# Kernel optimization log

Measured on AMD Instinct MI355X. Metric: run time of the kernel, lower is better.

Reference implementation:

```python
import jax, jax.numpy as jnp
import numpy as np

D_MODEL = 1024
NUM_HEADS = 16
DILATION = 2
SEGMENT = 2048


def setup_inputs() -> dict:
    key = jax.random.key(0)
    ks = jax.random.split(key, 5)
    B, S, D = 2, 8192, D_MODEL
    scale = 1.0 / np.sqrt(D)
    return {
        "x": jax.random.normal(ks[0], (B, S, D), dtype=jnp.float32),
        "Wqkv": jax.random.normal(ks[1], (D, 3 * D), dtype=jnp.float32) * scale,
        "bqkv": jax.random.normal(ks[2], (3 * D,), dtype=jnp.float32) * 0.01,
        "Wout": jax.random.normal(ks[3], (D, D), dtype=jnp.float32) * scale,
        "bout": jax.random.normal(ks[4], (D,), dtype=jnp.float32) * 0.01,
    }


def reference(x, Wqkv, bqkv, Wout, bout):
    B, S, D = x.shape
    H = NUM_HEADS
    hd = D // H
    n_seg = S // SEGMENT
    # view into segments, then dilated strided token selection within each segment
    xs = x.reshape(B, n_seg, SEGMENT, D)[:, :, ::DILATION, :]  # [B, n_seg, L, D]
    L = xs.shape[2]
    # fused QKV projection (FlashMHA)
    qkv = xs @ Wqkv + bqkv                                      # [B, n_seg, L, 3D]
    qkv = qkv.reshape(B, n_seg, L, 3, H, hd)
    q, k, v = qkv[..., 0, :, :], qkv[..., 1, :, :], qkv[..., 2, :, :]
    scores = jnp.einsum("bsqhd,bskhd->bshqk", q, k) / jnp.sqrt(jnp.asarray(hd, x.dtype))
    probs = jax.nn.softmax(scores, axis=-1)                     # [B, n_seg, H, L, L]
    ctx = jnp.einsum("bshqk,bskhd->bsqhd", probs, v)            # [B, n_seg, L, H, hd]
    ctx = ctx.reshape(B, n_seg, L, D)
    out = ctx @ Wout + bout                                     # [B, n_seg, L, D]
    # dropout p=0, casual=False, no rel-pos bias -> identity here
    return out.reshape(B, n_seg * L, D)                         # [B, S // DILATION, D]
```

## Files before the change

kernel.cpp:

```cpp
#include <hip/hip_runtime.h>
#include <hip/hip_bf16.h>

#define TOKENS  8192
#define QK_SC2  0.1803368801f

typedef short  short8 __attribute__((ext_vector_type(8)));
typedef float  f32x4  __attribute__((ext_vector_type(4)));
typedef float  f32x16 __attribute__((ext_vector_type(16)));
typedef unsigned short us4 __attribute__((ext_vector_type(4)));

__device__ __forceinline__ unsigned short f2bf_rne(float f) {
    unsigned u = __float_as_uint(f);
    unsigned r = (u + 0x7FFFu + ((u >> 16) & 1u)) >> 16;
    return (unsigned short)r;
}
__device__ __forceinline__ unsigned cvt_pk_bf16(float a, float b) {
    unsigned r;
    asm("v_cvt_pk_bf16_f32 %0, %1, %2" : "=v"(r) : "v"(a), "v"(b));
    return r;
}
__device__ __forceinline__ void permlane32_swap(unsigned &a, unsigned &b) {
    asm("v_permlane32_swap_b32 %0, %1" : "+v"(a), "+v"(b));
}
__device__ __forceinline__ void gld16(const void* gptr, void* lptr) {
    __builtin_amdgcn_global_load_lds(
        (const __attribute__((address_space(1))) void*)gptr,
        (__attribute__((address_space(3))) void*)lptr, 16, 0, 0);
}

__global__ __launch_bounds__(256)
void prep_x_kernel(const float* __restrict__ x, unsigned short* __restrict__ Ax)
{
    const int t = blockIdx.x;
    const int c = threadIdx.x * 4;
    const long xrow = (long)((t >> 10) * 2048 + (t & 1023) * 2);
    float4 v = *reinterpret_cast<const float4*>(&x[xrow * 1024 + c]);
    us4 hv;
    hv[0] = f2bf_rne(v.x);
    hv[1] = f2bf_rne(v.y);
    hv[2] = f2bf_rne(v.z);
    hv[3] = f2bf_rne(v.w);
    *reinterpret_cast<us4*>(&Ax[(size_t)t * 1024 + c]) = hv;
}

__global__ __launch_bounds__(256)
void prep_w_kernel(const float* __restrict__ W, unsigned short* __restrict__ Wt, int N)
{
    __shared__ float T[32][33];
    const int n0 = blockIdx.x * 32, k0 = blockIdx.y * 32;
    const int tid = threadIdx.x;
#pragma unroll
    for (int p = 0; p < 4; p++) {
        int r = p * 8 + (tid >> 5), c = tid & 31;
        T[r][c] = W[(long)(k0 + r) * N + n0 + c];
    }
    __syncthreads();
#pragma unroll
    for (int p = 0; p < 4; p++) {
        int on = p * 8 + (tid >> 5), ok = tid & 31;
        Wt[(size_t)(n0 + on) * 1024 + k0 + ok] = f2bf_rne(T[ok][on]);
    }
}

template<int EPI, int ASPLIT>
__global__ __launch_bounds__(512, 1)
void gemm2p_kernel(const unsigned short* __restrict__ A,
                   const unsigned short* __restrict__ Bt,
                   const float* __restrict__ bias,
                   float* __restrict__ C,
                   unsigned short* __restrict__ Qb,
                   unsigned short* __restrict__ Kb,
                   unsigned short* __restrict__ Vt,
                   int N, int NBX)
{
    __shared__ __align__(16) char lds[3 * 49152];

    const int NT = ASPLIT ? 32 : 16;
    const int ASTRIDE = ASPLIT ? 2048 : 1024;

    const int tid = threadIdx.x;
    const int l = tid & 63, w = tid >> 6;
    const int wm = w >> 2, wn = w & 3;
    const int l15 = l & 15;

    const int cpx = gridDim.x >> 3;
    const int wg = (blockIdx.x & 7) * cpx + (blockIdx.x >> 3);
    const int by = wg / NBX, bx = wg - by * NBX;
    const int trow0 = by * 128, col0 = bx * 256;

    size_t gOff[6];
    int    lOff[6];
    {
        const int c = tid & 7;
#pragma unroll
        for (int p = 0; p < 2; p++) {
            {
                const int row = (tid + p * 512) >> 3;
                const int cg = c ^ (row & 7);
                gOff[p] = (size_t)(trow0 + row) * ASTRIDE + cg * 8;
                lOff[p] = row * 128 + c * 16;
            }
            {
                const int u = (tid + p * 512) >> 3;
                const int row = ((u >> 5) << 6) + (u & 31);
                const int cg = c ^ (row & 7);
                gOff[2 + p] = (size_t)(col0 + row) * 1024 + cg * 8;
                lOff[2 + p] = 16384 + row * 128 + c * 16;
            }
            {
                const int u = (tid + p * 512) >> 3;
                const int row = ((u >> 5) << 6) + 32 + (u & 31);
                const int cg = c ^ (row & 7);
                gOff[4 + p] = (size_t)(col0 + row) * 1024 + cg * 8;
                lOff[4 + p] = 16384 + row * 128 + c * 16;
            }
        }
    }

    const int offs0 = (((l >> 4) * 16)     ) ^ ((l & 7) << 4);
    const int offs1 = (((l >> 4) * 16) + 64) ^ ((l & 7) << 4);

    f32x4 acc[4][4];
#pragma unroll
    for (int i = 0; i < 4; i++)
#pragma unroll
        for (int j = 0; j < 4; j++) acc[i][j] = (f32x4){0.f, 0.f, 0.f, 0.f};

#pragma unroll
    for (int t0 = 0; t0 < 2; ++t0) {
        char* buf = lds + t0 * 49152;
        const int ac = t0 * 64;
        gld16(&A [gOff[0] + ac], buf + lOff[0]);
        gld16(&A [gOff[1] + ac], buf + lOff[1]);
        gld16(&Bt[gOff[2] + ac], buf + lOff[2]);
        gld16(&Bt[gOff[3] + ac], buf + lOff[3]);
        gld16(&Bt[gOff[4] + ac], buf + lOff[4]);
        gld16(&Bt[gOff[5] + ac], buf + lOff[5]);
    }
    asm volatile("s_waitcnt vmcnt(6)" ::: "memory");
    __builtin_amdgcn_s_barrier();

    int bc3 = 0;
    for (int t = 0; t < NT; ++t) {
        char* buf = lds + bc3 * 49152;
        const int bn = (bc3 >= 1) ? bc3 - 1 : 2;
        char* nbuf = lds + bn * 49152;
        const int tp = t + 2;
        const bool pf = (tp < NT);
        const int ac  = pf ? (ASPLIT ? (((tp >> 4) ? 1024 : 0) + (tp & 15) * 64)
                                     : tp * 64) : 0;
        const int bcc = pf ? ((tp & 15) * 64) : 0;

        short8 af[4][2], bf0[2][2], bf1[2][2];
#pragma unroll
        for (int i = 0; i < 4; ++i) {
            const int r = wm * 64 + i * 16 + l15;
            af[i][0] = *reinterpret_cast<const short8*>(buf + r * 128 + offs0);
            af[i][1] = *reinterpret_cast<const short8*>(buf + r * 128 + offs1);
        }
#pragma unroll
        for (int j = 0; j < 2; ++j) {
            const int r = wn * 64 + j * 16 + l15;
            bf0[j][0] = *reinterpret_cast<const short8*>(buf + 16384 + r * 128 + offs0);
            bf0[j][1] = *reinterpret_cast<const short8*>(buf + 16384 + r * 128 + offs1);
        }
        if (pf) {
            gld16(&A [gOff[0] + ac],  nbuf + lOff[0]);
            gld16(&A [gOff[1] + ac],  nbuf + lOff[1]);
            gld16(&Bt[gOff[2] + bcc], nbuf + lOff[2]);
            gld16(&Bt[gOff[3] + bcc], nbuf + lOff[3]);
        }
        __builtin_amdgcn_s_barrier();
        __builtin_amdgcn_s_setprio(1);
#pragma unroll
        for (int i = 0; i < 4; ++i)
#pragma unroll
            for (int j = 0; j < 2; ++j) {
                acc[i][j] = __builtin_amdgcn_mfma_f32_16x16x32_bf16(
                    af[i][0], bf0[j][0], acc[i][j], 0, 0, 0);
                acc[i][j] = __builtin_amdgcn_mfma_f32_16x16x32_bf16(
                    af[i][1], bf0[j][1], acc[i][j], 0, 0, 0);
            }
        __builtin_amdgcn_s_setprio(0);
        __builtin_amdgcn_s_barrier();

#pragma unroll
        for (int j = 0; j < 2; ++j) {
            const int r = wn * 64 + 32 + j * 16 + l15;
            bf1[j][0] = *reinterpret_cast<const short8*>(buf + 16384 + r * 128 + offs0);
            bf1[j][1] = *reinterpret_cast<const short8*>(buf + 16384 + r * 128 + offs1);
        }
        if (pf) {
            gld16(&Bt[gOff[4] + bcc], nbuf + lOff[4]);
            gld16(&Bt[gOff[5] + bcc], nbuf + lOff[5]);
        }
        __builtin_amdgcn_s_barrier();
        __builtin_amdgcn_s_setprio(1);
#pragma unroll
        for (int i = 0; i < 4; ++i)
#pragma unroll
            for (int j = 0; j < 2; ++j) {
                acc[i][2 + j] = __builtin_amdgcn_mfma_f32_16x16x32_bf16(
                    af[i][0], bf1[j][0], acc[i][2 + j], 0, 0, 0);
                acc[i][2 + j] = __builtin_amdgcn_mfma_f32_16x16x32_bf16(
                    af[i][1], bf1[j][1], acc[i][2 + j], 0, 0, 0);
            }
        __builtin_amdgcn_s_setprio(0);

        if (pf) asm volatile("s_waitcnt vmcnt(6)" ::: "memory");
        else    asm volatile("s_waitcnt vmcnt(0)" ::: "memory");
        __builtin_amdgcn_s_barrier();

        bc3 = (bc3 >= 2) ? 0 : bc3 + 1;
    }

#pragma unroll
    for (int j = 0; j < 4; ++j) {
        const int gc = col0 + wn * 64 + j * 16 + l15;
        const float bv = bias[gc];
        if (EPI == 0) {
#pragma unroll
            for (int i = 0; i < 4; ++i) {
                const int gr0 = trow0 + wm * 64 + i * 16 + (l >> 4) * 4;
#pragma unroll
                for (int r = 0; r < 4; ++r)
                    C[(size_t)(gr0 + r) * N + gc] = acc[i][j][r] + bv;
            }
        } else {
            const int which = gc >> 10;
            const int head  = (gc >> 6) & 15;
            const int d     = gc & 63;
            if (which == 2) {
#pragma unroll
                for (int i = 0; i < 4; ++i) {
                    const int gr0 = trow0 + wm * 64 + i * 16 + (l >> 4) * 4;
                    const size_t base =
                        ((size_t)((gr0 >> 10) * 16 + head) << 16)
                        + (size_t)d * 1024 + (gr0 & 1023);
                    union { unsigned u[2]; us4 v; } pk;
                    pk.u[0] = cvt_pk_bf16(acc[i][j][0] + bv, acc[i][j][1] + bv);
                    pk.u[1] = cvt_pk_bf16(acc[i][j][2] + bv, acc[i][j][3] + bv);
                    *reinterpret_cast<us4*>(&Vt[base]) = pk.v;
                }
            } else {
                unsigned short* dst = (which == 0) ? Qb : Kb;
                const float sc = (which == 0) ? QK_SC2 : 1.f;
#pragma unroll
                for (int i = 0; i < 4; ++i) {
                    const int gr0 = trow0 + wm * 64 + i * 16 + (l >> 4) * 4;
                    const unsigned a01 = cvt_pk_bf16((acc[i][j][0] + bv) * sc,
                                                     (acc[i][j][1] + bv) * sc);
                    const unsigned a23 = cvt_pk_bf16((acc[i][j][2] + bv) * sc,
                                                     (acc[i][j][3] + bv) * sc);
                    const size_t adr0 = ((size_t)((gr0 >> 10) * 16 + head) << 16)
                                      + (size_t)(gr0 & 1023) * 64 + d;
                    dst[adr0]           = (unsigned short)a01;
                    dst[adr0 + 64]      = (unsigned short)(a01 >> 16);
                    dst[adr0 + 128]     = (unsigned short)a23;
                    dst[adr0 + 192]     = (unsigned short)(a23 >> 16);
                }
            }
        }
    }
}

__global__ __launch_bounds__(256)
void attn_mfma_kernel(const unsigned short* __restrict__ Qb,
                      const unsigned short* __restrict__ Kb,
                      const unsigned short* __restrict__ Vt,
                      unsigned short* __restrict__ ctx)
{
    __shared__ __align__(16) char Ks[2][8192];
    __shared__ __align__(16) char Vs[2][8192];

    const int id  = blockIdx.x;
    const int bsh = (id >> 6) * 8 + (id & 7);
    const int qc  = (id >> 3) & 7;
    const int bseg = bsh >> 4, h = bsh & 15;
    const int tid = threadIdx.x;
    const int w = tid >> 6, l = tid & 63;
    const int H = l >> 5, lq = l & 31;
    const int q0 = qc * 128 + w * 32;

    const size_t hbytes = (size_t)bsh << 17;

    int srowA[2], scolA[2], sdst[2];
#pragma unroll
    for (int p = 0; p < 2; p++) {
        const int c = w + p * 4;
        const int o = c * 1024 + l * 16;
        srowA[p] = o >> 7;
        scolA[p] = (o & 127) ^ ((l >> 3) << 4);
        sdst[p]  = c * 1024;
    }

    short8 qf[4];
    {
        const char* qsrc = (const char*)Qb + hbytes + (size_t)(q0 + lq) * 128;
#pragma unroll
        for (int ks = 0; ks < 4; ks++)
            qf[ks] = *reinterpret_cast<const short8*>(qsrc + ks * 32 + H * 16);
    }

    f32x16 o0, o1;
#pragma unroll
    for (int r = 0; r < 16; r++) { o0[r] = 0.f; o1[r] = 0.f; }
    float lsum = 0.f;

#pragma unroll
    for (int p = 0; p < 2; p++) {
        gld16((const char*)Kb + hbytes + (size_t)(srowA[p]) * 128 + scolA[p],
              Ks[0] + sdst[p]);
        gld16((const char*)Vt + hbytes + (size_t)srowA[p] * 2048 + scolA[p],
              Vs[0] + sdst[p]);
    }
    __syncthreads();

    for (int t = 0; t < 16; t++) {
        const int cur = t & 1;

        if (t + 1 < 16) {
            const int nb = cur ^ 1;
#pragma unroll
            for (int p = 0; p < 2; p++) {
                gld16((const char*)Kb + hbytes
                          + (size_t)((t + 1) * 64 + srowA[p]) * 128 + scolA[p],
                      Ks[nb] + sdst[p]);
                gld16((const char*)Vt + hbytes
                          + (size_t)srowA[p] * 2048 + (t + 1) * 128 + scolA[p],
                      Vs[nb] + sdst[p]);
            }
        }

        f32x16 s0, s1;
#pragma unroll
        for (int r = 0; r < 16; r++) { s0[r] = 0.f; s1[r] = 0.f; }
#pragma unroll
        for (int ks = 0; ks < 4; ks++) {
            const int b0 = (lq * 128 + ks * 32 + H * 16) ^ ((lq & 7) << 4);
            short8 k0 = *reinterpret_cast<const short8*>(Ks[cur] + b0);
            short8 k1 = *reinterpret_cast<const short8*>(Ks[cur] + b0 + 4096);
            s0 = __builtin_amdgcn_mfma_f32_32x32x16_bf16(k0, qf[ks], s0, 0, 0, 0);
            s1 = __builtin_amdgcn_mfma_f32_32x32x16_bf16(k1, qf[ks], s1, 0, 0, 0);
        }

        float pv[32];
        float ps = 0.f;
#pragma unroll
        for (int r = 0; r < 16; r++) {
            pv[r]      = __builtin_amdgcn_exp2f(s0[r]);
            pv[16 + r] = __builtin_amdgcn_exp2f(s1[r]);
        }
#pragma unroll
        for (int r = 0; r < 32; r++) ps += pv[r];
        lsum += ps;

#pragma unroll
        for (int kf = 0; kf < 2; kf++) {
            unsigned c8[8];
#pragma unroll
            for (int i = 0; i < 8; i++)
                c8[i] = cvt_pk_bf16(pv[kf * 16 + 2 * i], pv[kf * 16 + 2 * i + 1]);
#pragma unroll
            for (int tt = 0; tt < 2; tt++) {
                const int b = tt * 4;
                unsigned u0 = c8[b + 0], u2 = c8[b + 2];
                unsigned u1 = c8[b + 1], u3 = c8[b + 3];
                permlane32_swap(u0, u2);
                permlane32_swap(u1, u3);
                union { unsigned u[4]; short8 v; } pa;
                pa.u[0] = u0; pa.u[1] = u1; pa.u[2] = u2; pa.u[3] = u3;
                const int vb0 = (lq * 128 + kf * 64 + tt * 32 + H * 16) ^ ((lq & 7) << 4);
                short8 v0 = *reinterpret_cast<const short8*>(Vs[cur] + vb0);
                short8 v1 = *reinterpret_cast<const short8*>(Vs[cur] + vb0 + 4096);
                o0 = __builtin_amdgcn_mfma_f32_32x32x16_bf16(pa.v, v0, o0, 0, 0, 0);
                o1 = __builtin_amdgcn_mfma_f32_32x32x16_bf16(pa.v, v1, o1, 0, 0, 0);
            }
        }

        if (t + 1 < 16) __syncthreads();
    }

    const float lt = lsum + __shfl_xor(lsum, 32);
#pragma unroll
    for (int r = 0; r < 16; r++) {
        const int qrow = (r & 3) + 8 * (r >> 2) + 4 * H;
        const float inv = 1.f / __shfl(lt, qrow);
        const size_t tok = (size_t)bseg * 1024 + q0 + qrow;
        unsigned short* p0 = ctx + tok * 1024 + h * 64 + lq;
        const unsigned pk = cvt_pk_bf16(o0[r] * inv, o1[r] * inv);
        p0[0]  = (unsigned short)pk;
        p0[32] = (unsigned short)(pk >> 16);
    }
}

extern "C" void kernel_launch(void* const* d_in, const int* in_sizes, int n_in,
                              void* d_out, int out_size, void* d_ws, size_t ws_size,
                              hipStream_t stream)
{
    const float* x    = (const float*)d_in[0];
    const float* Wqkv = (const float*)d_in[1];
    const float* bqkv = (const float*)d_in[2];
    const float* Wout = (const float*)d_in[3];
    const float* bout = (const float*)d_in[4];
    float* out = (float*)d_out;

    char* ws = (char*)d_ws;
    unsigned short* Ax  = (unsigned short*)(ws);
    unsigned short* Wqt = (unsigned short*)(ws + 33554432);
    unsigned short* Wot = (unsigned short*)(ws + 46137344);
    unsigned short* Qb  = (unsigned short*)(ws + 50331648);
    unsigned short* Kb  = (unsigned short*)(ws + 67108864);
    unsigned short* Vt  = (unsigned short*)(ws + 100663296);
    unsigned short* ctx = (unsigned short*)(ws + 117440512);

    prep_x_kernel<<<TOKENS, 256, 0, stream>>>(x, Ax);
    prep_w_kernel<<<dim3(96, 32), 256, 0, stream>>>(Wqkv, Wqt, 3072);
    prep_w_kernel<<<dim3(32, 32), 256, 0, stream>>>(Wout, Wot, 1024);

    gemm2p_kernel<1, 0><<<768, 512, 0, stream>>>(
        Ax, Wqt, bqkv, (float*)nullptr, Qb, Kb, Vt, 3072, 12);

    attn_mfma_kernel<<<1024, 256, 0, stream>>>(Qb, Kb, Vt, ctx);

    gemm2p_kernel<0, 0><<<256, 512, 0, stream>>>(
        ctx, Wot, bout, out, (unsigned short*)nullptr,
        (unsigned short*)nullptr, (unsigned short*)nullptr, 1024, 4);
}
```

Baseline: 157.0 us.

## Process two query sub-tiles per wave in attention and merge weight prep launches

The attention kernel now gives each wave 64 query rows (two 32-row sub-tiles) instead of 32. K and V fragments are loaded from shared memory once per tile and reused for both sub-tiles, which halves the grid and the global K/V traffic per query. The two weight-conversion kernels are merged into a single launch to remove one launch. The cost is more registers per wave from the doubled accumulators and Q fragments, which may lower occupancy, and fewer blocks (512) to spread across the CUs.

```diff
diff --git a/kernel.cpp b/kernel.cpp
--- a/kernel.cpp
+++ b/kernel.cpp
@@ -44,10 +44,17 @@
 }
 
 __global__ __launch_bounds__(256)
-void prep_w_kernel(const float* __restrict__ W, unsigned short* __restrict__ Wt, int N)
+void prep_w2_kernel(const float* __restrict__ Wq, const float* __restrict__ Wo,
+                    unsigned short* __restrict__ Wqt, unsigned short* __restrict__ Wot)
 {
     __shared__ float T[32][33];
-    const int n0 = blockIdx.x * 32, k0 = blockIdx.y * 32;
+    const int bx = blockIdx.x;
+    const float* W;
+    unsigned short* Wt;
+    int N, n0;
+    if (bx < 96) { W = Wq; Wt = Wqt; N = 3072; n0 = bx * 32; }
+    else         { W = Wo; Wt = Wot; N = 1024; n0 = (bx - 96) * 32; }
+    const int k0 = blockIdx.y * 32;
     const int tid = threadIdx.x;
 #pragma unroll
     for (int p = 0; p < 4; p++) {
@@ -274,13 +281,13 @@
     __shared__ __align__(16) char Vs[2][8192];
 
     const int id  = blockIdx.x;
-    const int bsh = (id >> 6) * 8 + (id & 7);
-    const int qc  = (id >> 3) & 7;
+    const int bsh = (id >> 5) * 8 + (id & 7);
+    const int qc  = (id >> 3) & 3;
     const int bseg = bsh >> 4, h = bsh & 15;
     const int tid = threadIdx.x;
     const int w = tid >> 6, l = tid & 63;
     const int H = l >> 5, lq = l & 31;
-    const int q0 = qc * 128 + w * 32;
+    const int q0 = qc * 256 + w * 64;
 
     const size_t hbytes = (size_t)bsh << 17;
 
@@ -294,18 +301,24 @@
         sdst[p]  = c * 1024;
     }
 
-    short8 qf[4];
-    {
-        const char* qsrc = (const char*)Qb + hbytes + (size_t)(q0 + lq) * 128;
+    short8 qf[2][4];
+#pragma unroll
+    for (int qs = 0; qs < 2; qs++) {
+        const char* qsrc = (const char*)Qb + hbytes
+                         + (size_t)(q0 + qs * 32 + lq) * 128;
 #pragma unroll
         for (int ks = 0; ks < 4; ks++)
-            qf[ks] = *reinterpret_cast<const short8*>(qsrc + ks * 32 + H * 16);
-    }
-
-    f32x16 o0, o1;
-#pragma unroll
-    for (int r = 0; r < 16; r++) { o0[r] = 0.f; o1[r] = 0.f; }
-    float lsum = 0.f;
+            qf[qs][ks] = *reinterpret_cast<const short8*>(qsrc + ks * 32 + H * 16);
+    }
+
+    f32x16 acc[2][2];
+#pragma unroll
+    for (int qs = 0; qs < 2; qs++)
+#pragma unroll
+        for (int vh = 0; vh < 2; vh++)
+#pragma unroll
+            for (int r = 0; r < 16; r++) acc[qs][vh][r] = 0.f;
+    float lsum0 = 0.f, lsum1 = 0.f;
 
 #pragma unroll
     for (int p = 0; p < 2; p++) {
@@ -332,65 +345,90 @@
             }
         }
 
-        f32x16 s0, s1;
-#pragma unroll
-        for (int r = 0; r < 16; r++) { s0[r] = 0.f; s1[r] = 0.f; }
+        short8 kfr[4][2];
 #pragma unroll
         for (int ks = 0; ks < 4; ks++) {
             const int b0 = (lq * 128 + ks * 32 + H * 16) ^ ((lq & 7) << 4);
-            short8 k0 = *reinterpret_cast<const short8*>(Ks[cur] + b0);
-            short8 k1 = *reinterpret_cast<const short8*>(Ks[cur] + b0 + 4096);
-            s0 = __builtin_amdgcn_mfma_f32_32x32x16_bf16(k0, qf[ks], s0, 0, 0, 0);
-            s1 = __builtin_amdgcn_mfma_f32_32x32x16_bf16(k1, qf[ks], s1, 0, 0, 0);
-        }
-
-        float pv[32];
-        float ps = 0.f;
+            kfr[ks][0] = *reinterpret_cast<const short8*>(Ks[cur] + b0);
+            kfr[ks][1] = *reinterpret_cast<const short8*>(Ks[cur] + b0 + 4096);
+        }
+        short8 vfr[2][2][2];
+#pragma unroll
+        for (int kf = 0; kf < 2; kf++)
+#pragma unroll
+            for (int tt = 0; tt < 2; tt++) {
+                const int vb0 = (lq * 128 + kf * 64 + tt * 32 + H * 16)
+                              ^ ((lq & 7) << 4);
+                vfr[kf][tt][0] = *reinterpret_cast<const short8*>(Vs[cur] + vb0);
+                vfr[kf][tt][1] = *reinterpret_cast<const short8*>(Vs[cur] + vb0 + 4096);
+            }
+
+#pragma unroll
+        for (int qs = 0; qs < 2; qs++) {
+            f32x16 s0, s1;
+#pragma unroll
+            for (int r = 0; r < 16; r++) { s0[r] = 0.f; s1[r] = 0.f; }
+#pragma unroll
+            for (int ks = 0; ks < 4; ks++) {
+                s0 = __builtin_amdgcn_mfma_f32_32x32x16_bf16(
+                    kfr[ks][0], qf[qs][ks], s0, 0, 0, 0);
+                s1 = __builtin_amdgcn_mfma_f32_32x32x16_bf16(
+                    kfr[ks][1], qf[qs][ks], s1, 0, 0, 0);
+            }
+
+            float pv[32];
+            float ps = 0.f;
+#pragma unroll
+            for (int r = 0; r < 16; r++) {
+                pv[r]      = __builtin_amdgcn_exp2f(s0[r]);
+                pv[16 + r] = __builtin_amdgcn_exp2f(s1[r]);
+            }
+#pragma unroll
+            for (int r = 0; r < 32; r++) ps += pv[r];
+            if (qs == 0) lsum0 += ps; else lsum1 += ps;
+
+#pragma unroll
+            for (int kf = 0; kf < 2; kf++) {
+                unsigned c8[8];
+#pragma unroll
+                for (int i = 0; i < 8; i++)
+                    c8[i] = cvt_pk_bf16(pv[kf * 16 + 2 * i],
+                                        pv[kf * 16 + 2 * i + 1]);
+#pragma unroll
+                for (int tt = 0; tt < 2; tt++) {
+                    const int b = tt * 4;
+                    unsigned u0 = c8[b + 0], u2 = c8[b + 2];
+                    unsigned u1 = c8[b + 1], u3 = c8[b + 3];
+                    permlane32_swap(u0, u2);
+                    permlane32_swap(u1, u3);
+                    union { unsigned u[4]; short8 v; } pa;
+                    pa.u[0] = u0; pa.u[1] = u1; pa.u[2] = u2; pa.u[3] = u3;
+                    acc[qs][0] = __builtin_amdgcn_mfma_f32_32x32x16_bf16(
+                        pa.v, vfr[kf][tt][0], acc[qs][0], 0, 0, 0);
+                    acc[qs][1] = __builtin_amdgcn_mfma_f32_32x32x16_bf16(
+                        pa.v, vfr[kf][tt][1], acc[qs][1], 0, 0, 0);
+                }
+            }
+        }
+
+        if (t + 1 < 16) __syncthreads();
+    }
+
+#pragma unroll
+    for (int qs = 0; qs < 2; qs++) {
+        const float ls = (qs == 0) ? lsum0 : lsum1;
+        const float lt = ls + __shfl_xor(ls, 32);
 #pragma unroll
         for (int r = 0; r < 16; r++) {
-            pv[r]      = __builtin_amdgcn_exp2f(s0[r]);
-            pv[16 + r] = __builtin_amdgcn_exp2f(s1[r]);
-        }
-#pragma unroll
-        for (int r = 0; r < 32; r++) ps += pv[r];
-        lsum += ps;
-
-#pragma unroll
-        for (int kf = 0; kf < 2; kf++) {
-            unsigned c8[8];
-#pragma unroll
-            for (int i = 0; i < 8; i++)
-                c8[i] = cvt_pk_bf16(pv[kf * 16 + 2 * i], pv[kf * 16 + 2 * i + 1]);
-#pragma unroll
-            for (int tt = 0; tt < 2; tt++) {
-                const int b = tt * 4;
-                unsigned u0 = c8[b + 0], u2 = c8[b + 2];
-                unsigned u1 = c8[b + 1], u3 = c8[b + 3];
-                permlane32_swap(u0, u2);
-                permlane32_swap(u1, u3);
-                union { unsigned u[4]; short8 v; } pa;
-                pa.u[0] = u0; pa.u[1] = u1; pa.u[2] = u2; pa.u[3] = u3;
-                const int vb0 = (lq * 128 + kf * 64 + tt * 32 + H * 16) ^ ((lq & 7) << 4);
-                short8 v0 = *reinterpret_cast<const short8*>(Vs[cur] + vb0);
-                short8 v1 = *reinterpret_cast<const short8*>(Vs[cur] + vb0 + 4096);
-                o0 = __builtin_amdgcn_mfma_f32_32x32x16_bf16(pa.v, v0, o0, 0, 0, 0);
-                o1 = __builtin_amdgcn_mfma_f32_32x32x16_bf16(pa.v, v1, o1, 0, 0, 0);
-            }
-        }
-
-        if (t + 1 < 16) __syncthreads();
-    }
-
-    const float lt = lsum + __shfl_xor(lsum, 32);
-#pragma unroll
-    for (int r = 0; r < 16; r++) {
-        const int qrow = (r & 3) + 8 * (r >> 2) + 4 * H;
-        const float inv = 1.f / __shfl(lt, qrow);
-        const size_t tok = (size_t)bseg * 1024 + q0 + qrow;
-        unsigned short* p0 = ctx + tok * 1024 + h * 64 + lq;
-        const unsigned pk = cvt_pk_bf16(o0[r] * inv, o1[r] * inv);
-        p0[0]  = (unsigned short)pk;
-        p0[32] = (unsigned short)(pk >> 16);
+            const int qrow = (r & 3) + 8 * (r >> 2) + 4 * H;
+            const float inv = 1.f / __shfl(lt, qrow);
+            const size_t tok = (size_t)bseg * 1024 + q0 + qs * 32 + qrow;
+            unsigned short* p0 = ctx + tok * 1024 + h * 64 + lq;
+            const unsigned pk = cvt_pk_bf16(acc[qs][0][r] * inv,
+                                            acc[qs][1][r] * inv);
+            p0[0]  = (unsigned short)pk;
+            p0[32] = (unsigned short)(pk >> 16);
+        }
     }
 }
 
@@ -415,13 +453,12 @@
     unsigned short* ctx = (unsigned short*)(ws + 117440512);
 
     prep_x_kernel<<<TOKENS, 256, 0, stream>>>(x, Ax);
-    prep_w_kernel<<<dim3(96, 32), 256, 0, stream>>>(Wqkv, Wqt, 3072);
-    prep_w_kernel<<<dim3(32, 32), 256, 0, stream>>>(Wout, Wot, 1024);
+    prep_w2_kernel<<<dim3(128, 32), 256, 0, stream>>>(Wqkv, Wout, Wqt, Wot);
 
     gemm2p_kernel<1, 0><<<768, 512, 0, stream>>>(
         Ax, Wqt, bqkv, (float*)nullptr, Qb, Kb, Vt, 3072, 12);
 
-    attn_mfma_kernel<<<1024, 256, 0, stream>>>(Qb, Kb, Vt, ctx);
+    attn_mfma_kernel<<<512, 256, 0, stream>>>(Qb, Kb, Vt, ctx);
 
     gemm2p_kernel<0, 0><<<256, 512, 0, stream>>>(
         ctx, Wot, bout, out, (unsigned short*)nullptr,
```

Result: slower. 169.3 us (+7.8%).
